# Kernel optimization log

Measured on AMD Instinct MI355X. Metric: run time of the kernel, lower is better.

Reference implementation:

```python
import jax, jax.numpy as jnp
import numpy as np

N_NODES = 100000
N_EDGES = 1600000
F_IN = 128
HID = 64
EPS = 1e-5


def setup_inputs() -> dict:
    key = jax.random.key(0)
    ks = jax.random.split(key, 16)
    x = jax.random.normal(ks[0], (N_NODES, F_IN), dtype=jnp.float32)
    edge_index = jax.random.randint(ks[1], (2, N_EDGES), 0, N_NODES, dtype=jnp.int64)
    inp = {"x": x, "edge_index": edge_index}
    # GCN layers: layer 0 maps F_IN->HID, layers 1,2 map HID->HID
    dims = [(F_IN, HID), (HID, HID), (HID, HID)]
    for i, (fi, fo) in enumerate(dims):
        inp[f"W{i}"] = jax.random.normal(ks[2 + i], (fi, fo), dtype=jnp.float32) / np.sqrt(fi)
        inp[f"b{i}"] = jnp.zeros((fo,), dtype=jnp.float32)
        inp[f"g{i}"] = jnp.ones((fo,), dtype=jnp.float32)
        inp[f"bt{i}"] = jnp.zeros((fo,), dtype=jnp.float32)
    inp["lw1"] = jax.random.normal(ks[8], (HID, HID // 2), dtype=jnp.float32) / np.sqrt(HID)
    inp["lb1"] = jnp.zeros((HID // 2,), dtype=jnp.float32)
    inp["lw2"] = jax.random.normal(ks[9], (HID // 2, 1), dtype=jnp.float32) / np.sqrt(HID // 2)
    inp["lb2"] = jnp.zeros((1,), dtype=jnp.float32)
    return inp


def _gcn_norm(edge_index, n_nodes):
    # add self loops, symmetric normalization D^{-1/2}(A+I)D^{-1/2}
    loops = jnp.arange(n_nodes, dtype=edge_index.dtype)
    src = jnp.concatenate([edge_index[0], loops])
    dst = jnp.concatenate([edge_index[1], loops])
    deg = jax.ops.segment_sum(jnp.ones_like(dst, dtype=jnp.float32), dst, num_segments=n_nodes)
    dinv = jax.lax.rsqrt(deg)  # deg >= 1 thanks to self loops
    norm = dinv[src] * dinv[dst]  # [E+N]
    return src, dst, norm


def reference(x, edge_index, W0, b0, g0, bt0, W1, b1, g1, bt1, W2, b2, g2, bt2, lw1, lb1, lw2, lb2):
    n = x.shape[0]
    src, dst, norm = _gcn_norm(edge_index, n)
    layers = [(W0, b0, g0, bt0), (W1, b1, g1, bt1), (W2, b2, g2, bt2)]
    h = x
    for W, b, g, bt in layers:
        hw = h @ W                                  # [N, H] dense GEMM
        msg = hw[src] * norm[:, None]               # gather + scale, [E+N, H]
        agg = jax.ops.segment_sum(msg, dst, num_segments=n) + b  # scatter-add
        # BatchNorm1d (training-mode batch stats, biased var)
        mu = agg.mean(axis=0)
        var = agg.var(axis=0)
        h = (agg - mu) * jax.lax.rsqrt(var + EPS) * g + bt
        h = jax.nn.relu(h)                          # dropout = identity (inference)
    h = jax.nn.relu(h @ lw1 + lb1)
    out = h @ lw2 + lb2                             # [N, 1]
    return out[:, 0]
```

## Files before the change

### kernel.cpp

```cpp
#include <hip/hip_runtime.h>
#include <hip/hip_fp16.h>

#define HIDW 64
#define EPSV 1e-5f
#define CAP 32
#define NPART 8
#define SLOTS 64
#define NSLOT 64
#define OVFCAP 65536

__global__ __launch_bounds__(256) void k_zero(int* __restrict__ deg, int* __restrict__ ovfcnt,
                                              float* __restrict__ stats, int n) {
    int i = blockIdx.x * 256 + threadIdx.x;
    if (i < n) deg[i] = 0;
    if (i == 0) ovfcnt[0] = 0;
    if (i < 3 * NSLOT * 128) stats[i] = 0.f;
}

__global__ __launch_bounds__(256) void k_part(const int* __restrict__ srcv, const int* __restrict__ dstv,
                                              int2* __restrict__ pairs, unsigned char* __restrict__ cnts,
                                              int* __restrict__ deg, int* __restrict__ csr,
                                              int2* __restrict__ ovfl, int* __restrict__ ovfcnt,
                                              int e, int nchunk) {
    __shared__ int lcnt[NPART];
    int tid = threadIdx.x;
    int chunk = blockIdx.x;
    if (tid < NPART) lcnt[tid] = 0;
    __syncthreads();
    int i = chunk * 256 + tid;
    bool valid = (i < e);
    int s = 0, d = 0, k = 0, slot = 0;
    if (valid) {
        s = srcv[i];
        d = dstv[i];
        k = (d >> 10) & (NPART - 1);
        slot = atomicAdd(&lcnt[k], 1);
    }
    __syncthreads();
    if (valid) {
        if (slot < SLOTS) {
            pairs[((size_t)k * nchunk + chunk) * SLOTS + slot] = make_int2(s, d);
        } else {
            int bslot = atomicAdd(&deg[d], 1);
            if (bslot < CAP) {
                csr[(size_t)d * CAP + bslot] = s;
            } else {
                int o = atomicAdd(ovfcnt, 1);
                if (o < OVFCAP) ovfl[o] = make_int2(s, d);
            }
        }
    }
    if (tid < NPART) cnts[chunk * NPART + tid] = (unsigned char)min(lcnt[tid], SLOTS);
}

__global__ __launch_bounds__(256) void k_bucket(const int2* __restrict__ pairs, const unsigned char* __restrict__ cnts,
                                                int* __restrict__ deg, int* __restrict__ csr,
                                                int2* __restrict__ ovfl, int* __restrict__ ovfcnt, int nchunk) {
    int part = blockIdx.x & (NPART - 1);
    int grp = blockIdx.x >> 3;
    int w = threadIdx.x >> 6;
    int lane = threadIdx.x & 63;
    int chunk = grp * 4 + w;
    if (chunk >= nchunk) return;
    int cnt = cnts[chunk * NPART + part];
    if (lane >= cnt) return;
    int2 p = pairs[((size_t)part * nchunk + chunk) * SLOTS + lane];
    int slot = atomicAdd(&deg[p.y], 1);
    if (slot < CAP) {
        csr[(size_t)p.y * CAP + slot] = p.x;
    } else {
        int o = atomicAdd(ovfcnt, 1);
        if (o < OVFCAP) ovfl[o] = p;
    }
}

__global__ __launch_bounds__(256) void k_ovf(const __half* __restrict__ hw, const int2* __restrict__ ovfl,
                                             const int* __restrict__ ovfcnt, const int* __restrict__ deg,
                                             float* __restrict__ agg) {
    int m = min(ovfcnt[0], OVFCAP);
    if (m == 0) return;
    int lane = threadIdx.x & 63;
    int w = (blockIdx.x * 256 + threadIdx.x) >> 6;
    for (; w < m; w += gridDim.x * 4) {
        int2 p = ovfl[w];
        float wt = rsqrtf(1.0f + (float)deg[p.y]);
        atomicAdd(&agg[(size_t)p.y * HIDW + lane], __half2float(hw[(size_t)p.x * HIDW + lane]) * wt);
    }
}

__global__ __launch_bounds__(256) void k_count(const int* __restrict__ dstv, int* __restrict__ deg, int e) {
    int i = blockIdx.x * 256 + threadIdx.x;
    if (i < e) atomicAdd(&deg[dstv[i]], 1);
}

__global__ __launch_bounds__(256) void k_scan1(const int* __restrict__ deg, int* __restrict__ off,
                                               int* __restrict__ bsum, int n) {
    __shared__ int s[256];
    int tid = threadIdx.x;
    int i = blockIdx.x * 256 + tid;
    int v = (i < n) ? deg[i] : 0;
    s[tid] = v;
    __syncthreads();
    for (int o = 1; o < 256; o <<= 1) {
        int t = (tid >= o) ? s[tid - o] : 0;
        __syncthreads();
        s[tid] += t;
        __syncthreads();
    }
    if (i < n) off[i] = s[tid] - v;
    if (tid == 255) bsum[blockIdx.x] = s[255];
}

__global__ __launch_bounds__(512) void k_scan2(int* __restrict__ bsum, int nb) {
    __shared__ int s[512];
    int tid = threadIdx.x;
    int v = (tid < nb) ? bsum[tid] : 0;
    s[tid] = v;
    __syncthreads();
    for (int o = 1; o < 512; o <<= 1) {
        int t = (tid >= o) ? s[tid - o] : 0;
        __syncthreads();
        s[tid] += t;
        __syncthreads();
    }
    if (tid < nb) bsum[tid] = s[tid] - v;
}

__global__ __launch_bounds__(256) void k_scan3(int* __restrict__ off, const int* __restrict__ bsum, int n) {
    int i = blockIdx.x * 256 + threadIdx.x;
    if (i < n) off[i] += bsum[blockIdx.x];
}

__global__ __launch_bounds__(256) void k_fill2(const int* __restrict__ srcv, const int* __restrict__ dstv,
                                               int* __restrict__ roff, int* __restrict__ csr, int e) {
    int i = blockIdx.x * 256 + threadIdx.x;
    if (i < e) {
        int d = dstv[i];
        int p = atomicAdd(&roff[d], 1);
        csr[p] = srcv[i];
    }
}

template <int K, bool BN>
__global__ __launch_bounds__(256) void k_gemm(const float* __restrict__ h, const float* __restrict__ W,
                                              __half* __restrict__ hw, int n,
                                              const float* __restrict__ st, const float* __restrict__ g,
                                              const float* __restrict__ bt, float invn,
                                              const int* __restrict__ deg) {
    constexpr int KP = K + 4;
    constexpr int KQ = K / 4;
    __shared__ float sH[64 * KP];
    __shared__ float sW[K * 64];
    __shared__ float sM[128];
    __shared__ float sSc[HIDW];
    __shared__ float sSh[HIDW];
    int tid = threadIdx.x;
    int node0 = blockIdx.x * 64;

    if (BN) {
        if (tid < 128) {
            float t = 0.f;
#pragma unroll 8
            for (int s = 0; s < NSLOT; ++s) t += st[s * 128 + tid];
            sM[tid] = t;
        }
        __syncthreads();
        if (tid < HIDW) {
            float mu = sM[tid] * invn;
            float var = sM[HIDW + tid] * invn - mu * mu;
            var = fmaxf(var, 0.f);
            float rstd = rsqrtf(var + EPSV);
            float sc = rstd * g[tid];
            sSc[tid] = sc;
            sSh[tid] = bt[tid] - mu * sc;
        }
        __syncthreads();
    }

    for (int i = tid; i < K * 16; i += 256)
        ((float4*)sW)[i] = ((const float4*)W)[i];
    for (int i = tid; i < 64 * KQ; i += 256) {
        int row = i / KQ, kq = i % KQ;
        int nn = node0 + row;
        if (nn >= n) nn = n - 1;
        float4 v = ((const float4*)h)[(size_t)nn * KQ + kq];
        if (BN) {
            int c = 4 * kq;
            v.x = fmaxf(fmaf(v.x, sSc[c + 0], sSh[c + 0]), 0.f);
            v.y = fmaxf(fmaf(v.y, sSc[c + 1], sSh[c + 1]), 0.f);
            v.z = fmaxf(fmaf(v.z, sSc[c + 2], sSh[c + 2]), 0.f);
            v.w = fmaxf(fmaf(v.w, sSc[c + 3], sSh[c + 3]), 0.f);
        }
        ((float4*)(sH + row * KP))[kq] = v;
    }
    __syncthreads();

    int tx = tid & 15;
    int ny = tid >> 4;
    const float* hbase = sH + (4 * ny) * KP;

    float acc[4][4];
#pragma unroll
    for (int j = 0; j < 4; ++j)
#pragma unroll
        for (int c = 0; c < 4; ++c) acc[j][c] = 0.f;

#pragma unroll 2
    for (int kq = 0; kq < KQ; ++kq) {
        float4 w0 = ((const float4*)(sW + (4 * kq + 0) * 64))[tx];
        float4 w1 = ((const float4*)(sW + (4 * kq + 1) * 64))[tx];
        float4 w2 = ((const float4*)(sW + (4 * kq + 2) * 64))[tx];
        float4 w3 = ((const float4*)(sW + (4 * kq + 3) * 64))[tx];
#pragma unroll
        for (int j = 0; j < 4; ++j) {
            float4 hv = ((const float4*)(hbase + j * KP))[kq];
            acc[j][0] = fmaf(hv.x, w0.x, acc[j][0]);
            acc[j][1] = fmaf(hv.x, w0.y, acc[j][1]);
            acc[j][2] = fmaf(hv.x, w0.z, acc[j][2]);
            acc[j][3] = fmaf(hv.x, w0.w, acc[j][3]);
            acc[j][0] = fmaf(hv.y, w1.x, acc[j][0]);
            acc[j][1] = fmaf(hv.y, w1.y, acc[j][1]);
            acc[j][2] = fmaf(hv.y, w1.z, acc[j][2]);
            acc[j][3] = fmaf(hv.y, w1.w, acc[j][3]);
            acc[j][0] = fmaf(hv.z, w2.x, acc[j][0]);
            acc[j][1] = fmaf(hv.z, w2.y, acc[j][1]);
            acc[j][2] = fmaf(hv.z, w2.z, acc[j][2]);
            acc[j][3] = fmaf(hv.z, w2.w, acc[j][3]);
            acc[j][0] = fmaf(hv.w, w3.x, acc[j][0]);
            acc[j][1] = fmaf(hv.w, w3.y, acc[j][1]);
            acc[j][2] = fmaf(hv.w, w3.z, acc[j][2]);
            acc[j][3] = fmaf(hv.w, w3.w, acc[j][3]);
        }
    }

#pragma unroll
    for (int j = 0; j < 4; ++j) {
        int node = node0 + 4 * ny + j;
        if (node < n) {
            float dv = rsqrtf(1.0f + (float)deg[node]);
            __half2 p01 = __floats2half2_rn(acc[j][0] * dv, acc[j][1] * dv);
            __half2 p23 = __floats2half2_rn(acc[j][2] * dv, acc[j][3] * dv);
            uint2 r;
            r.x = *(unsigned int*)&p01;
            r.y = *(unsigned int*)&p23;
            ((uint2*)hw)[(size_t)node * 16 + tx] = r;
        }
    }
}

template <bool BUCKET>
__global__ __launch_bounds__(256) void k_gather(const __half* __restrict__ hw, const int* __restrict__ csr,
                                                const int* __restrict__ roff, const int* __restrict__ deg,
                                                const float* __restrict__ bias,
                                                float* __restrict__ agg, float* __restrict__ st, int n) {
    __shared__ float sS[4 * 64];
    __shared__ float sQ[4 * 64];
    int tid = threadIdx.x;
    int lane = tid & 63;
    int w = tid >> 6;
    int eh = lane >> 5;
    int c2 = lane & 31;
    int v = blockIdx.x * 4 + w;
    bool valid = (v < n);
    int vv = valid ? v : 0;
    int dcnt = deg[vv];
    float dv = rsqrtf(1.0f + (float)dcnt);
    int cnt;
    const int* base;
    if (BUCKET) {
        cnt = min(dcnt, CAP);
        base = csr + (size_t)vv * CAP;
    } else {
        cnt = dcnt;
        base = csr + (roff[vv] - dcnt);
    }
    const __half2* hw2 = (const __half2*)hw;
    float2 acc;
    {
        float2 f = __half22float2(hw2[(size_t)vv * 32 + c2]);
        acc = (eh == 0) ? f : make_float2(0.f, 0.f);
    }
    for (int j0 = 0; j0 < cnt; j0 += 64) {
        int m = min(cnt - j0, 64);
        int idx = (lane < m) ? base[j0 + lane] : 0;
        int nfull = m >> 1;
        int p = 0;
        for (; p + 4 <= nfull; p += 4) {
            int a0 = __shfl(idx, 2 * (p + 0) + eh);
            int a1 = __shfl(idx, 2 * (p + 1) + eh);
            int a2 = __shfl(idx, 2 * (p + 2) + eh);
            int a3 = __shfl(idx, 2 * (p + 3) + eh);
            float2 f0 = __half22float2(hw2[(size_t)a0 * 32 + c2]);
            float2 f1 = __half22float2(hw2[(size_t)a1 * 32 + c2]);
            float2 f2 = __half22float2(hw2[(size_t)a2 * 32 + c2]);
            float2 f3 = __half22float2(hw2[(size_t)a3 * 32 + c2]);
            acc.x += (f0.x + f1.x) + (f2.x + f3.x);
            acc.y += (f0.y + f1.y) + (f2.y + f3.y);
        }
        for (; p < nfull; ++p) {
            int a = __shfl(idx, 2 * p + eh);
            float2 f = __half22float2(hw2[(size_t)a * 32 + c2]);
            acc.x += f.x;
            acc.y += f.y;
        }
        if (m & 1) {
            int a = __shfl(idx, m - 1);
            float2 f = __half22float2(hw2[(size_t)a * 32 + c2]);
            if (eh == 0) {
                acc.x += f.x;
                acc.y += f.y;
            }
        }
    }
    acc.x += __shfl_xor(acc.x, 32);
    acc.y += __shfl_xor(acc.y, 32);
    float2 b2 = ((const float2*)bias)[c2];
    float2 fin;
    fin.x = fmaf(dv, acc.x, b2.x);
    fin.y = fmaf(dv, acc.y, b2.y);
    if (valid && eh == 0) ((float2*)agg)[(size_t)vv * 32 + c2] = fin;
    if (eh == 0) {
        float sx = valid ? fin.x : 0.f;
        float sy = valid ? fin.y : 0.f;
        sS[w * 64 + 2 * c2 + 0] = sx;
        sS[w * 64 + 2 * c2 + 1] = sy;
        sQ[w * 64 + 2 * c2 + 0] = sx * sx;
        sQ[w * 64 + 2 * c2 + 1] = sy * sy;
    }
    __syncthreads();
    if (tid < 64) {
        float S = sS[tid] + sS[64 + tid] + sS[128 + tid] + sS[192 + tid];
        float Q = sQ[tid] + sQ[64 + tid] + sQ[128 + tid] + sQ[192 + tid];
        float* slot = st + (size_t)(blockIdx.x & (NSLOT - 1)) * 128;
        atomicAdd(&slot[tid], S);
        atomicAdd(&slot[64 + tid], Q);
    }
}

__global__ __launch_bounds__(256) void k_head(const float* __restrict__ h, const float* __restrict__ lw1,
                                              const float* __restrict__ lb1, const float* __restrict__ lw2,
                                              const float* __restrict__ lb2, float* __restrict__ out, int n,
                                              const float* __restrict__ st, const float* __restrict__ g,
                                              const float* __restrict__ bt, float invn) {
    __shared__ float sW[64 * 32];
    __shared__ float sb1[32];
    __shared__ float sw2[32];
    __shared__ float sM[128];
    __shared__ float sSc[HIDW];
    __shared__ float sSh[HIDW];
    int tid = threadIdx.x;
    for (int i = tid; i < 64 * 32; i += 256) sW[i] = lw1[i];
    if (tid < 32) {
        sb1[tid] = lb1[tid];
        sw2[tid] = lw2[tid];
    }
    if (tid < 128) {
        float t = 0.f;
#pragma unroll 8
        for (int s = 0; s < NSLOT; ++s) t += st[s * 128 + tid];
        sM[tid] = t;
    }
    __syncthreads();
    if (tid < HIDW) {
        float mu = sM[tid] * invn;
        float var = sM[HIDW + tid] * invn - mu * mu;
        var = fmaxf(var, 0.f);
        float rstd = rsqrtf(var + EPSV);
        float sc = rstd * g[tid];
        sSc[tid] = sc;
        sSh[tid] = bt[tid] - mu * sc;
    }
    __syncthreads();
    int nd = blockIdx.x * 256 + tid;
    if (nd >= n) return;
    float acc[32];
#pragma unroll
    for (int j = 0; j < 32; ++j) acc[j] = sb1[j];
    const float4* hr = (const float4*)(h + (size_t)nd * HIDW);
#pragma unroll 4
    for (int kc = 0; kc < 16; ++kc) {
        float4 h4 = hr[kc];
        int c = 4 * kc;
        h4.x = fmaxf(fmaf(h4.x, sSc[c + 0], sSh[c + 0]), 0.f);
        h4.y = fmaxf(fmaf(h4.y, sSc[c + 1], sSh[c + 1]), 0.f);
        h4.z = fmaxf(fmaf(h4.z, sSc[c + 2], sSh[c + 2]), 0.f);
        h4.w = fmaxf(fmaf(h4.w, sSc[c + 3], sSh[c + 3]), 0.f);
        const float* w0 = &sW[(c + 0) * 32];
        const float* w1 = &sW[(c + 1) * 32];
        const float* w2 = &sW[(c + 2) * 32];
        const float* w3 = &sW[(c + 3) * 32];
#pragma unroll
        for (int j = 0; j < 32; ++j) {
            float t = fmaf(h4.x, w0[j], fmaf(h4.y, w1[j], fmaf(h4.z, w2[j], h4.w * w3[j])));
            acc[j] += t;
        }
    }
    float o = lb2[0];
#pragma unroll
    for (int j = 0; j < 32; ++j) o = fmaf(fmaxf(acc[j], 0.f), sw2[j], o);
    out[nd] = o;
}

extern "C" void kernel_launch(void* const* d_in, const int* in_sizes, int n_in,
                              void* d_out, int out_size, void* d_ws, size_t ws_size,
                              hipStream_t stream) {
    const float* x = (const float*)d_in[0];
    const int* ei = (const int*)d_in[1];
    const float* W[3] = {(const float*)d_in[2], (const float*)d_in[6], (const float*)d_in[10]};
    const float* B[3] = {(const float*)d_in[3], (const float*)d_in[7], (const float*)d_in[11]};
    const float* G[3] = {(const float*)d_in[4], (const float*)d_in[8], (const float*)d_in[12]};
    const float* BT[3] = {(const float*)d_in[5], (const float*)d_in[9], (const float*)d_in[13]};
    const float* lw1 = (const float*)d_in[14];
    const float* lb1 = (const float*)d_in[15];
    const float* lw2 = (const float*)d_in[16];
    const float* lb2 = (const float*)d_in[17];
    float* out = (float*)d_out;

    const int n = in_sizes[0] / 128;
    const int e = in_sizes[1] / 2;
    const int* srcv = ei;
    const int* dstv = ei + e;
    const float invn = 1.0f / (float)n;
    const int nchunk = (e + 255) / 256;

    char* ws = (char*)d_ws;
    size_t off = 0;
    auto alloc = [&](size_t bytes) -> char* {
        off = (off + 511) & ~(size_t)511;
        char* p = ws + off;
        off += bytes;
        return p;
    };
    float* stats = (float*)alloc((size_t)3 * NSLOT * 128 * 4);
    int* ovfcnt = (int*)alloc(512);
    int2* ovfl = (int2*)alloc((size_t)OVFCAP * 8);
    unsigned char* cnts = (unsigned char*)alloc((size_t)nchunk * NPART);
    int* deg = (int*)alloc((size_t)n * 4);
    float* bufA = (float*)alloc((size_t)n * HIDW * 4);
    __half* bufB = (__half*)alloc((size_t)n * HIDW * 2);
    size_t commonOff = off;

    size_t needA = ((commonOff + 511) & ~(size_t)511) + (size_t)n * CAP * 4;
    bool useA = (needA <= ws_size) && ((size_t)NPART * nchunk * SLOTS * 8 <= (size_t)n * HIDW * 4);

    const int gN = (n + 255) / 256;
    const int gE = nchunk;
    const int gG = (n + 63) / 64;
    const int gV = (n + 3) / 4;

    int2* pairs = (int2*)bufA;
    int* csrB = nullptr;
    int* roff = nullptr;
    int* bsum = nullptr;
    int* csrC = nullptr;

    if (useA) {
        csrB = (int*)alloc((size_t)n * CAP * 4);
        k_zero<<<gN, 256, 0, stream>>>(deg, ovfcnt, stats, n);
        k_part<<<gE, 256, 0, stream>>>(srcv, dstv, pairs, cnts, deg, csrB, ovfl, ovfcnt, e, nchunk);
        int ngrp = (nchunk + 3) / 4;
        k_bucket<<<ngrp * NPART, 256, 0, stream>>>(pairs, cnts, deg, csrB, ovfl, ovfcnt, nchunk);
    } else {
        roff = (int*)alloc((size_t)(n + 1) * 4);
        bsum = (int*)alloc(512 * 4);
        csrC = (int*)alloc((size_t)e * 4);
        k_zero<<<gN, 256, 0, stream>>>(deg, ovfcnt, stats, n);
        k_count<<<(e + 255) / 256, 256, 0, stream>>>(dstv, deg, e);
        k_scan1<<<gN, 256, 0, stream>>>(deg, roff, bsum, n);
        k_scan2<<<1, 512, 0, stream>>>(bsum, gN);
        k_scan3<<<gN, 256, 0, stream>>>(roff, bsum, n);
        k_fill2<<<(e + 255) / 256, 256, 0, stream>>>(srcv, dstv, roff, csrC, e);
    }

    for (int L = 0; L < 3; ++L) {
        float* stL = stats + (size_t)L * NSLOT * 128;
        if (L == 0)
            k_gemm<128, false><<<gG, 256, 0, stream>>>(x, W[0], bufB, n, nullptr, nullptr, nullptr, invn, deg);
        else
            k_gemm<64, true><<<gG, 256, 0, stream>>>(bufA, W[L], bufB, n, stats + (size_t)(L - 1) * NSLOT * 128,
                                                     G[L - 1], BT[L - 1], invn, deg);
        if (useA) {
            k_gather<true><<<gV, 256, 0, stream>>>(bufB, csrB, nullptr, deg, B[L], bufA, stL, n);
            k_ovf<<<16, 256, 0, stream>>>(bufB, ovfl, ovfcnt, deg, bufA);
        } else {
            k_gather<false><<<gV, 256, 0, stream>>>(bufB, csrC, roff, deg, B[L], bufA, stL, n);
        }
    }

    k_head<<<gN, 256, 0, stream>>>(bufA, lw1, lb1, lw2, lb2, out, n, stats + (size_t)2 * NSLOT * 128,
                                   G[2], BT[2], invn);
}
```

Measured before the change: 431.9 us.

## Build bucketed CSR per node-group in shared memory instead of global atomics

Edge partitioning now bins edges by 512-node destination groups, using 4096-edge chunks and a fixed number of slots per bin and chunk. A new per-group kernel then scatters each group's edges into an LDS bucket table with shared atomics. It writes the CSR rows, degrees and a byte-sized clamped count to global memory in one coalesced pass. This replaces global-memory atomicAdd on deg and scattered csr writes, with a small extra kernel to fold partition-overflow edges into degrees. The trade-off is only ~196 blocks with large LDS footprints in the build step, and the gather now reads a separate count array.

```diff
diff --git a/kernel.cpp b/kernel.cpp
--- a/kernel.cpp
+++ b/kernel.cpp
@@ -4,85 +4,111 @@
 #define HIDW 64
 #define EPSV 1e-5f
 #define CAP 32
-#define NPART 8
-#define SLOTS 64
+#define GRP 512
+#define CHUNK 4096
+#define PSLOTS 40
+#define NBIN_MAX 256
+#define NCHUNK_MAX 512
 #define NSLOT 64
-#define OVFCAP 65536
+#define OVFR 32768
 
 __global__ __launch_bounds__(256) void k_zero(int* __restrict__ deg, int* __restrict__ ovfcnt,
                                               float* __restrict__ stats, int n) {
     int i = blockIdx.x * 256 + threadIdx.x;
     if (i < n) deg[i] = 0;
-    if (i == 0) ovfcnt[0] = 0;
+    if (i < 2) ovfcnt[i] = 0;
     if (i < 3 * NSLOT * 128) stats[i] = 0.f;
 }
 
 __global__ __launch_bounds__(256) void k_part(const int* __restrict__ srcv, const int* __restrict__ dstv,
                                               int2* __restrict__ pairs, unsigned char* __restrict__ cnts,
-                                              int* __restrict__ deg, int* __restrict__ csr,
                                               int2* __restrict__ ovfl, int* __restrict__ ovfcnt,
-                                              int e, int nchunk) {
-    __shared__ int lcnt[NPART];
+                                              int e, int nchunk, int nbin) {
+    __shared__ int lcnt[NBIN_MAX];
     int tid = threadIdx.x;
     int chunk = blockIdx.x;
-    if (tid < NPART) lcnt[tid] = 0;
-    __syncthreads();
-    int i = chunk * 256 + tid;
-    bool valid = (i < e);
-    int s = 0, d = 0, k = 0, slot = 0;
-    if (valid) {
-        s = srcv[i];
-        d = dstv[i];
-        k = (d >> 10) & (NPART - 1);
-        slot = atomicAdd(&lcnt[k], 1);
-    }
-    __syncthreads();
-    if (valid) {
-        if (slot < SLOTS) {
-            pairs[((size_t)k * nchunk + chunk) * SLOTS + slot] = make_int2(s, d);
-        } else {
-            int bslot = atomicAdd(&deg[d], 1);
-            if (bslot < CAP) {
-                csr[(size_t)d * CAP + bslot] = s;
+    for (int i = tid; i < nbin; i += 256) lcnt[i] = 0;
+    __syncthreads();
+    int base = chunk * CHUNK;
+#pragma unroll
+    for (int t = 0; t < CHUNK / 256; ++t) {
+        int i = base + t * 256 + tid;
+        if (i < e) {
+            int s = srcv[i];
+            int d = dstv[i];
+            int k = d >> 9;
+            int slot = atomicAdd(&lcnt[k], 1);
+            if (slot < PSLOTS) {
+                pairs[((size_t)k * nchunk + chunk) * PSLOTS + slot] = make_int2(s, d);
             } else {
-                int o = atomicAdd(ovfcnt, 1);
-                if (o < OVFCAP) ovfl[o] = make_int2(s, d);
+                int o = atomicAdd(&ovfcnt[0], 1);
+                if (o < OVFR) ovfl[o] = make_int2(s, d);
             }
         }
     }
-    if (tid < NPART) cnts[chunk * NPART + tid] = (unsigned char)min(lcnt[tid], SLOTS);
-}
-
-__global__ __launch_bounds__(256) void k_bucket(const int2* __restrict__ pairs, const unsigned char* __restrict__ cnts,
-                                                int* __restrict__ deg, int* __restrict__ csr,
-                                                int2* __restrict__ ovfl, int* __restrict__ ovfcnt, int nchunk) {
-    int part = blockIdx.x & (NPART - 1);
-    int grp = blockIdx.x >> 3;
-    int w = threadIdx.x >> 6;
-    int lane = threadIdx.x & 63;
-    int chunk = grp * 4 + w;
-    if (chunk >= nchunk) return;
-    int cnt = cnts[chunk * NPART + part];
-    if (lane >= cnt) return;
-    int2 p = pairs[((size_t)part * nchunk + chunk) * SLOTS + lane];
-    int slot = atomicAdd(&deg[p.y], 1);
-    if (slot < CAP) {
-        csr[(size_t)p.y * CAP + slot] = p.x;
-    } else {
-        int o = atomicAdd(ovfcnt, 1);
-        if (o < OVFCAP) ovfl[o] = p;
-    }
+    __syncthreads();
+    for (int i = tid; i < nbin; i += 256)
+        cnts[(size_t)i * nchunk + chunk] = (unsigned char)min(lcnt[i], PSLOTS);
+}
+
+__global__ __launch_bounds__(256) void k_own(const int2* __restrict__ pairs, const unsigned char* __restrict__ cnts,
+                                             int* __restrict__ deg, unsigned char* __restrict__ bcnt,
+                                             int* __restrict__ csr, int2* __restrict__ ovfl,
+                                             int* __restrict__ ovfcnt, int n, int nchunk) {
+    __shared__ int lcnt[GRP];
+    __shared__ int bkt[GRP * CAP];
+    __shared__ unsigned char scnt[NCHUNK_MAX];
+    int g = blockIdx.x;
+    int tid = threadIdx.x;
+    int nbase = g << 9;
+    int nloc = min(GRP, n - nbase);
+    for (int i = tid; i < GRP; i += 256) lcnt[i] = 0;
+    for (int i = tid; i < nchunk; i += 256) scnt[i] = cnts[(size_t)g * nchunk + i];
+    __syncthreads();
+    const int2* pb = pairs + (size_t)g * nchunk * PSLOTS;
+    int tot = nchunk * PSLOTS;
+    for (int i = tid; i < tot; i += 256) {
+        int c = i / PSLOTS;
+        int s = i - c * PSLOTS;
+        if (s < (int)scnt[c]) {
+            int2 p = pb[i];
+            int loc = p.y - nbase;
+            int pos = atomicAdd(&lcnt[loc], 1);
+            if (pos < CAP) {
+                bkt[loc * CAP + pos] = p.x;
+            } else {
+                int o = atomicAdd(&ovfcnt[1], 1);
+                if (o < OVFR) ovfl[OVFR + o] = p;
+            }
+        }
+    }
+    __syncthreads();
+    int* csrb = csr + (size_t)nbase * CAP;
+    for (int i = tid; i < nloc * CAP; i += 256) csrb[i] = bkt[i];
+    for (int i = tid; i < nloc; i += 256) {
+        int c = lcnt[i];
+        deg[nbase + i] = c;
+        bcnt[nbase + i] = (unsigned char)min(c, CAP);
+    }
+}
+
+__global__ __launch_bounds__(256) void k_ovfdeg(const int2* __restrict__ ovfl, const int* __restrict__ ovfcnt,
+                                                int* __restrict__ deg) {
+    int m0 = min(ovfcnt[0], OVFR);
+    for (int i = threadIdx.x; i < m0; i += 256) atomicAdd(&deg[ovfl[i].y], 1);
 }
 
 __global__ __launch_bounds__(256) void k_ovf(const __half* __restrict__ hw, const int2* __restrict__ ovfl,
                                              const int* __restrict__ ovfcnt, const int* __restrict__ deg,
                                              float* __restrict__ agg) {
-    int m = min(ovfcnt[0], OVFCAP);
-    if (m == 0) return;
+    int m0 = min(ovfcnt[0], OVFR);
+    int m1 = min(ovfcnt[1], OVFR);
+    int tot = m0 + m1;
+    if (tot == 0) return;
     int lane = threadIdx.x & 63;
     int w = (blockIdx.x * 256 + threadIdx.x) >> 6;
-    for (; w < m; w += gridDim.x * 4) {
-        int2 p = ovfl[w];
+    for (; w < tot; w += gridDim.x * 4) {
+        int2 p = (w < m0) ? ovfl[w] : ovfl[OVFR + (w - m0)];
         float wt = rsqrtf(1.0f + (float)deg[p.y]);
         atomicAdd(&agg[(size_t)p.y * HIDW + lane], __half2float(hw[(size_t)p.x * HIDW + lane]) * wt);
     }
@@ -251,6 +277,7 @@
 template <bool BUCKET>
 __global__ __launch_bounds__(256) void k_gather(const __half* __restrict__ hw, const int* __restrict__ csr,
                                                 const int* __restrict__ roff, const int* __restrict__ deg,
+                                                const unsigned char* __restrict__ bcnt,
                                                 const float* __restrict__ bias,
                                                 float* __restrict__ agg, float* __restrict__ st, int n) {
     __shared__ float sS[4 * 64];
@@ -268,7 +295,7 @@
     int cnt;
     const int* base;
     if (BUCKET) {
-        cnt = min(dcnt, CAP);
+        cnt = bcnt[vv];
         base = csr + (size_t)vv * CAP;
     } else {
         cnt = dcnt;
@@ -421,7 +448,8 @@
     const int* srcv = ei;
     const int* dstv = ei + e;
     const float invn = 1.0f / (float)n;
-    const int nchunk = (e + 255) / 256;
+    const int nchunk = (e + CHUNK - 1) / CHUNK;
+    const int nbin = (n + GRP - 1) / GRP;
 
     char* ws = (char*)d_ws;
     size_t off = 0;
@@ -433,18 +461,20 @@
     };
     float* stats = (float*)alloc((size_t)3 * NSLOT * 128 * 4);
     int* ovfcnt = (int*)alloc(512);
-    int2* ovfl = (int2*)alloc((size_t)OVFCAP * 8);
-    unsigned char* cnts = (unsigned char*)alloc((size_t)nchunk * NPART);
+    int2* ovfl = (int2*)alloc((size_t)2 * OVFR * 8);
+    unsigned char* cnts = (unsigned char*)alloc((size_t)nbin * nchunk);
+    unsigned char* bcnt = (unsigned char*)alloc((size_t)n);
     int* deg = (int*)alloc((size_t)n * 4);
     float* bufA = (float*)alloc((size_t)n * HIDW * 4);
     __half* bufB = (__half*)alloc((size_t)n * HIDW * 2);
     size_t commonOff = off;
 
     size_t needA = ((commonOff + 511) & ~(size_t)511) + (size_t)n * CAP * 4;
-    bool useA = (needA <= ws_size) && ((size_t)NPART * nchunk * SLOTS * 8 <= (size_t)n * HIDW * 4);
+    size_t pairsBytes = (size_t)nbin * nchunk * PSLOTS * 8;
+    bool useA = (needA <= ws_size) && (pairsBytes <= (size_t)n * HIDW * 4) &&
+                (nchunk <= NCHUNK_MAX) && (nbin <= NBIN_MAX);
 
     const int gN = (n + 255) / 256;
-    const int gE = nchunk;
     const int gG = (n + 63) / 64;
     const int gV = (n + 3) / 4;
 
@@ -457,9 +487,9 @@
     if (useA) {
         csrB = (int*)alloc((size_t)n * CAP * 4);
         k_zero<<<gN, 256, 0, stream>>>(deg, ovfcnt, stats, n);
-        k_part<<<gE, 256, 0, stream>>>(srcv, dstv, pairs, cnts, deg, csrB, ovfl, ovfcnt, e, nchunk);
-        int ngrp = (nchunk + 3) / 4;
-        k_bucket<<<ngrp * NPART, 256, 0, stream>>>(pairs, cnts, deg, csrB, ovfl, ovfcnt, nchunk);
+        k_part<<<nchunk, 256, 0, stream>>>(srcv, dstv, pairs, cnts, ovfl, ovfcnt, e, nchunk, nbin);
+        k_own<<<nbin, 256, 0, stream>>>(pairs, cnts, deg, bcnt, csrB, ovfl, ovfcnt, n, nchunk);
+        k_ovfdeg<<<1, 256, 0, stream>>>(ovfl, ovfcnt, deg);
     } else {
         roff = (int*)alloc((size_t)(n + 1) * 4);
         bsum = (int*)alloc(512 * 4);
@@ -480,10 +510,10 @@
             k_gemm<64, true><<<gG, 256, 0, stream>>>(bufA, W[L], bufB, n, stats + (size_t)(L - 1) * NSLOT * 128,
                                                      G[L - 1], BT[L - 1], invn, deg);
         if (useA) {
-            k_gather<true><<<gV, 256, 0, stream>>>(bufB, csrB, nullptr, deg, B[L], bufA, stL, n);
+            k_gather<true><<<gV, 256, 0, stream>>>(bufB, csrB, nullptr, deg, bcnt, B[L], bufA, stL, n);
             k_ovf<<<16, 256, 0, stream>>>(bufB, ovfl, ovfcnt, deg, bufA);
         } else {
-            k_gather<false><<<gV, 256, 0, stream>>>(bufB, csrC, roff, deg, B[L], bufA, stL, n);
+            k_gather<false><<<gV, 256, 0, stream>>>(bufB, csrC, roff, deg, nullptr, B[L], bufA, stL, n);
         }
     }
 
```

Result: faster. 404.4 us (-6.4%).
